# Performance work log

Hardware: AMD Instinct MI355X
Metric: run time of the kernel (lower is better)

Reference implementation:

```python
import jax, jax.numpy as jnp
import numpy as np

NUM_HEADS = 16
D_MODEL = 1024
HEAD_DIM = D_MODEL // NUM_HEADS  # 64
NEG_INF = -1e9


def alibi_bidirectional_bias(num_heads, seq_len, dtype=jnp.float32):
    """[num_heads, S, S] bias: first H/2 heads forward-causal ALiBi, last H/2 backward."""
    half = num_heads // 2
    base = 24.0 ** (1.0 / half)
    slopes = (1.0 / base ** jnp.arange(1, half + 1, dtype=dtype))[:, None, None]  # [half,1,1]
    pos = jnp.arange(seq_len)
    rel = (pos[None, :] - pos[:, None]).astype(dtype)  # rel[i,j] = j - i
    neg = jnp.full((seq_len, seq_len), NEG_INF, dtype=dtype)
    fwd = slopes * jnp.tril(rel) + jnp.triu(neg, 1)          # causal (attend past)
    bwd = slopes * jnp.triu(-rel) + jnp.tril(neg, -1)        # anti-causal (attend future)
    return jnp.concatenate([fwd, bwd], axis=0)  # [H, S, S]


def setup_inputs() -> dict:
    key = jax.random.key(0)
    ks = jax.random.split(key, 9)
    B, S, D = 2, 2048, D_MODEL
    sc = 1.0 / np.sqrt(D)
    inp = {"x": jax.random.normal(ks[0], (B, S, D), dtype=jnp.float32)}
    inp["Wq"] = jax.random.normal(ks[1], (D, D), dtype=jnp.float32) * sc
    inp["bq"] = jnp.zeros((D,), dtype=jnp.float32)
    inp["Wk"] = jax.random.normal(ks[2], (D, D), dtype=jnp.float32) * sc
    inp["bk"] = jnp.zeros((D,), dtype=jnp.float32)
    inp["Wv"] = jax.random.normal(ks[3], (D, D), dtype=jnp.float32) * sc
    inp["bv"] = jnp.zeros((D,), dtype=jnp.float32)
    inp["Wf"] = jax.random.normal(ks[4], (D, D), dtype=jnp.float32) * sc
    inp["bf"] = jnp.zeros((D,), dtype=jnp.float32)
    return inp


def reference(x, Wq, bq, Wk, bk, Wv, bv, Wf, bf):
    B, S, D = x.shape
    H, hd = NUM_HEADS, HEAD_DIM

    def heads(y):  # [B,S,D] -> [B,H,S,hd]
        return y.reshape(B, S, H, hd).transpose(0, 2, 1, 3)

    q = heads(x @ Wq + bq)
    k = heads(x @ Wk + bk)
    v = heads(x @ Wv + bv)

    bias = alibi_bidirectional_bias(H, S, x.dtype)  # [H,S,S]
    scores = jnp.einsum("bhqd,bhkd->bhqk", q, k) * (1.0 / np.sqrt(hd)) + bias[None]
    attn = jax.nn.softmax(scores, axis=-1)
    out = jnp.einsum("bhqk,bhkd->bhqd", attn, v)
    out = out.transpose(0, 2, 1, 3).reshape(B, S, D)
    return out @ Wf + bf
```

## Files before the change

kernel.cpp:

```cpp
#include <hip/hip_runtime.h>

#define S_LEN 2048
#define NH 16
#define HD 64
#define DM 1024
#define BSZ 2

typedef __bf16 bf16;
typedef __bf16 bf16x8 __attribute__((ext_vector_type(8)));
typedef float f32x4 __attribute__((ext_vector_type(4)));
typedef const unsigned int __attribute__((address_space(1)))* gas_ptr;
typedef unsigned int __attribute__((address_space(3)))* las_ptr;

__device__ __forceinline__ void gl_lds16(const bf16* g, bf16* l) {
  __builtin_amdgcn_global_load_lds((gas_ptr)g, (las_ptr)l, 16, 0, 0);
}

__global__ __launch_bounds__(256) void k_cast(const float* __restrict__ in,
                                              bf16* __restrict__ out, int n4) {
  int i = blockIdx.x * 256 + threadIdx.x;
  if (i >= n4) return;
  float4 v = ((const float4*)in)[i];
  union { ushort4 u; bf16 b[4]; } o;
  o.b[0] = (bf16)v.x; o.b[1] = (bf16)v.y; o.b[2] = (bf16)v.z; o.b[3] = (bf16)v.w;
  ((ushort4*)out)[i] = o.u;
}

__global__ __launch_bounds__(256) void k_transpose_w4(
    const float* __restrict__ W0, const float* __restrict__ W1,
    const float* __restrict__ W2, const float* __restrict__ W3,
    bf16* __restrict__ dqkv, bf16* __restrict__ df) {
  __shared__ float t[64][65];
  const int z = blockIdx.z;
  const float* W = (z == 0) ? W0 : (z == 1) ? W1 : (z == 2) ? W2 : W3;
  bf16* D = (z < 3) ? (dqkv + (size_t)z * 1048576) : df;
  int k0 = blockIdx.x * 64, n0 = blockIdx.y * 64;
  int c = threadIdx.x & 63, rr = threadIdx.x >> 6;
#pragma unroll
  for (int it = 0; it < 16; ++it) {
    int r = it * 4 + rr;
    t[r][c] = W[(size_t)(k0 + r) * DM + n0 + c];
  }
  __syncthreads();
#pragma unroll
  for (int it = 0; it < 16; ++it) {
    int r = it * 4 + rr;
    D[(size_t)(n0 + r) * DM + k0 + c] = (bf16)t[c][r];
  }
}

template <int MODE, int BM, int BN>
__global__ __launch_bounds__(256) void k_gemm(
    const bf16* __restrict__ A, const bf16* __restrict__ Bt,
    const float* __restrict__ b0, const float* __restrict__ b1,
    const float* __restrict__ b2, void* __restrict__ Cout,
    bf16* __restrict__ VtOut, int M, int N, int K) {
  __shared__ __align__(16) bf16 As[BM * 64];
  __shared__ __align__(16) bf16 Bs[BN * 64];
  constexpr int MIc = BM / 32, NIc = BN / 32;
  const int tid = threadIdx.x;
  const int l = tid & 63, w = tid >> 6;
  const int lm = l & 15, lg = l >> 4;
  const int bm = blockIdx.x * BM, bn = blockIdx.y * BN;
  const int wm = (w >> 1) * (BM / 2), wn = (w & 1) * (BN / 2);

  f32x4 acc[MIc][NIc] = {};
  const bf16* Ag = A + (size_t)bm * K;
  const bf16* Bg = Bt + (size_t)bn * K;

  for (int k0 = 0; k0 < K; k0 += 64) {
#pragma unroll
    for (int it = 0; it < BM / 32; ++it) {
      int cl = it * 256 + tid;
      int row = cl >> 3;
      int cs = ((cl & 7) ^ (row & 7)) << 3;
      gl_lds16(Ag + (size_t)row * K + k0 + cs, &As[(it * 256 + w * 64) * 8]);
    }
#pragma unroll
    for (int it = 0; it < BN / 32; ++it) {
      int cl = it * 256 + tid;
      int row = cl >> 3;
      int cs = ((cl & 7) ^ (row & 7)) << 3;
      gl_lds16(Bg + (size_t)row * K + k0 + cs, &Bs[(it * 256 + w * 64) * 8]);
    }
    __syncthreads();
#pragma unroll
    for (int kk = 0; kk < 2; ++kk) {
      bf16x8 af[MIc], bfr[NIc];
#pragma unroll
      for (int mi = 0; mi < MIc; ++mi) {
        int row = wm + mi * 16 + lm;
        af[mi] = *(const bf16x8*)&As[row * 64 + ((((kk << 2) + lg) ^ (row & 7)) << 3)];
      }
#pragma unroll
      for (int ni = 0; ni < NIc; ++ni) {
        int row = wn + ni * 16 + lm;
        bfr[ni] = *(const bf16x8*)&Bs[row * 64 + ((((kk << 2) + lg) ^ (row & 7)) << 3)];
      }
#pragma unroll
      for (int mi = 0; mi < MIc; ++mi)
#pragma unroll
        for (int ni = 0; ni < NIc; ++ni)
          acc[mi][ni] = __builtin_amdgcn_mfma_f32_16x16x32_bf16(
              af[mi], bfr[ni], acc[mi][ni], 0, 0, 0);
    }
    __syncthreads();
  }

#pragma unroll
  for (int ni = 0; ni < NIc; ++ni) {
    int n = bn + wn + ni * 16 + lm;
    float bv;
    if (MODE == 0) {
      const float* bp = (n < 1024) ? b0 : (n < 2048) ? b1 : b2;
      bv = bp[n & 1023];
    } else {
      bv = b0[n];
    }
#pragma unroll
    for (int mi = 0; mi < MIc; ++mi) {
#pragma unroll
      for (int r = 0; r < 4; ++r) {
        int m = bm + wm + mi * 16 + lg * 4 + r;
        float v = acc[mi][ni][r] + bv;
        if (MODE == 0) {
          int qkv = n >> 10;
          int h = (n >> 6) & 15;
          int d = n & 63;
          int b = m >> 11, s = m & 2047;
          if (qkv == 2) {
            VtOut[((size_t)(b * NH + h) * HD + d) * S_LEN + s] = (bf16)v;
          } else {
            ((bf16*)Cout)[(size_t)qkv * (BSZ * NH * S_LEN * HD) +
                          ((size_t)(b * NH + h) * S_LEN + s) * HD + d] = (bf16)v;
          }
        } else {
          ((float*)Cout)[(size_t)m * N + n] = v;
        }
      }
    }
  }
}

#define SMX(MASKED)                                                           \
  {                                                                           \
    const int dj = j0 - q0;                                                   \
    const float t0 = slp2 * (float)dj;                                        \
    _Pragma("unroll") for (int ni = 0; ni < 4; ++ni) {                        \
      const int koff = (ni & 1) * 32 + (ni >> 1) * 4;                         \
      float bni = t0 + dni[ni];                                               \
      float pr[4];                                                            \
      _Pragma("unroll") for (int r = 0; r < 4; ++r) {                         \
        float v = fmaf(sc[ni][r], c1, bni + srr[r]);                          \
        if (MASKED) {                                                         \
          int reli = dj + koff + relc + r;                                    \
          bool ok = causal ? (reli <= 0) : (reli >= 0);                       \
          v = ok ? v : -1e9f;                                                 \
        }                                                                     \
        pr[r] = __builtin_amdgcn_exp2f(v);                                    \
      }                                                                       \
      union { bf16 b[2]; unsigned u; } u0, u1;                                \
      u0.b[0] = (bf16)pr[0]; u0.b[1] = (bf16)pr[1];                           \
      u1.b[0] = (bf16)pr[2]; u1.b[1] = (bf16)pr[3];                           \
      pk[ni][0] = u0.u; pk[ni][1] = u1.u;                                     \
    }                                                                         \
  }

__device__ __forceinline__ void stage_kv(const bf16* __restrict__ Kp,
                                         const bf16* __restrict__ Vp,
                                         bf16* lk, bf16* lv, int j0,
                                         int w, int l) {
#pragma unroll
  for (int it = 0; it < 2; ++it) {
    const int clb = it * 256 + w * 64;
    const int cl = clb + l;
    const int row = cl >> 3, c = cl & 7;
    const int sw = (row & 3) | (((row >> 3) & 1) << 2);
    const int gc = (c ^ sw) << 3;
    gl_lds16(Kp + (size_t)(j0 + row) * HD + gc, lk + clb * 8);
    gl_lds16(Vp + (size_t)row * S_LEN + j0 + gc, lv + clb * 8);
  }
}

__global__ __launch_bounds__(256, 4) void k_attn(const bf16* __restrict__ Qh,
                                                 const bf16* __restrict__ Kh,
                                                 const bf16* __restrict__ Vt,
                                                 bf16* __restrict__ O) {
  __shared__ __align__(16) bf16 Ks[2][4096];
  __shared__ __align__(16) bf16 Vs[2][4096];
  const int id = blockIdx.x;
  const int g = id >> 3;
  const int bh = ((id & 7) << 2) | (g >> 5);
  const int yi = g & 31;
  const int b = bh >> 4, h = bh & 15;
  const bool causal = (h < 8);
  const int qb = (causal ? (31 - yi) : yi) * 64;
  const int nfull = 31 - yi;
  const int jf0 = causal ? 0 : qb + 64;
  const int w = threadIdx.x >> 6, l = threadIdx.x & 63;
  const int lm = l & 15, lg = l >> 4;
  const int q0 = qb + w * 16;
  const int hh = causal ? h : h - 8;
  const float c1 = 0.18033688f;
  const float sm = __builtin_amdgcn_exp2f(-(float)(hh + 1) * 0.57312035f) * 1.44269504f;
  const float slp2 = causal ? sm : -sm;
  const int relc = lg * 8 - lm;
  const int krow_lane = ((lm >> 2) << 3) + (lm & 3);
  const int swzK = (lm & 3) | (((lm >> 2) & 1) << 2);
  const int swzV = (lm & 3) | (((lm >> 3) & 1) << 2);
  float dni[4], srr[4];
#pragma unroll
  for (int ni = 0; ni < 4; ++ni)
    dni[ni] = slp2 * (float)((ni & 1) * 32 + (ni >> 1) * 4);
#pragma unroll
  for (int r = 0; r < 4; ++r) srr[r] = slp2 * (float)(relc + r);

  const bf16* Qp = Qh + (size_t)bh * S_LEN * HD;
  const bf16* Kp = Kh + (size_t)bh * S_LEN * HD;
  const bf16* Vp = Vt + (size_t)bh * HD * S_LEN;

  bf16x8 qf[2];
#pragma unroll
  for (int kk = 0; kk < 2; ++kk)
    qf[kk] = *(const bf16x8*)&Qp[(size_t)(q0 + lm) * HD + kk * 32 + lg * 8];
  bf16x8 ones;
#pragma unroll
  for (int i = 0; i < 8; ++i) ones[i] = (bf16)1.0f;

  f32x4 oacc[4] = {};
  f32x4 lacc = {};

  stage_kv(Kp, Vp, Ks[0], Vs[0], (0 < nfull) ? jf0 : qb, w, l);
  __syncthreads();

  for (int t = 0; t <= nfull; ++t) {
    const int cur = t & 1;
    if (t < nfull) {
      const int jn = (t + 1 < nfull) ? jf0 + (t + 1) * 64 : qb;
      stage_kv(Kp, Vp, Ks[cur ^ 1], Vs[cur ^ 1], jn, w, l);
    }
    const int j0 = (t < nfull) ? jf0 + t * 64 : qb;
    const bf16* lk = Ks[cur];
    const bf16* lv = Vs[cur];
    f32x4 sc[4] = {};
#pragma unroll
    for (int kk = 0; kk < 2; ++kk)
#pragma unroll
      for (int ni = 0; ni < 4; ++ni) {
        const int koff = (ni & 1) * 32 + (ni >> 1) * 4;
        bf16x8 kf = *(const bf16x8*)&lk[(koff + krow_lane) * 64 +
                                        ((((kk << 2) + lg) ^ swzK) << 3)];
        sc[ni] = __builtin_amdgcn_mfma_f32_16x16x32_bf16(kf, qf[kk], sc[ni], 0, 0, 0);
      }
    bf16x8 vf[2][4];
#pragma unroll
    for (int kk = 0; kk < 2; ++kk)
#pragma unroll
      for (int di = 0; di < 4; ++di)
        vf[kk][di] = *(const bf16x8*)&lv[(di * 16 + lm) * 64 +
                                         ((((kk << 2) + lg) ^ swzV) << 3)];
    unsigned pk[4][2];
    if (t == nfull) { SMX(true); } else { SMX(false); }
#pragma unroll
    for (int kk = 0; kk < 2; ++kk) {
      union { unsigned d[4]; bf16x8 v; } pa;
      pa.d[0] = pk[kk][0];
      pa.d[1] = pk[kk][1];
      pa.d[2] = pk[kk + 2][0];
      pa.d[3] = pk[kk + 2][1];
      lacc = __builtin_amdgcn_mfma_f32_16x16x32_bf16(pa.v, ones, lacc, 0, 0, 0);
#pragma unroll
      for (int di = 0; di < 4; ++di)
        oacc[di] = __builtin_amdgcn_mfma_f32_16x16x32_bf16(pa.v, vf[kk][di],
                                                           oacc[di], 0, 0, 0);
    }
    __syncthreads();
  }

  float rin[4];
#pragma unroll
  for (int r = 0; r < 4; ++r) rin[r] = 1.0f / lacc[r];
#pragma unroll
  for (int di = 0; di < 4; ++di) {
    int d = h * HD + di * 16 + lm;
#pragma unroll
    for (int r = 0; r < 4; ++r) {
      int q = q0 + lg * 4 + r;
      O[((size_t)b * S_LEN + q) * DM + d] = (bf16)(oacc[di][r] * rin[r]);
    }
  }
}

extern "C" void kernel_launch(void* const* d_in, const int* in_sizes, int n_in,
                              void* d_out, int out_size, void* d_ws, size_t ws_size,
                              hipStream_t stream) {
  const float* x  = (const float*)d_in[0];
  const float* Wq = (const float*)d_in[1];
  const float* bq = (const float*)d_in[2];
  const float* Wk = (const float*)d_in[3];
  const float* bk = (const float*)d_in[4];
  const float* Wv = (const float*)d_in[5];
  const float* bv = (const float*)d_in[6];
  const float* Wf = (const float*)d_in[7];
  const float* bfp = (const float*)d_in[8];

  char* ws = (char*)d_ws;
  const size_t MB = 1ull << 20;
  bf16* xb    = (bf16*)(ws);
  bf16* Wqkvt = (bf16*)(ws + 8 * MB);
  bf16* Wft   = (bf16*)(ws + 14 * MB);
  bf16* QKVh  = (bf16*)(ws + 16 * MB);
  bf16* Vt    = (bf16*)(ws + 40 * MB);
  bf16* O     = QKVh + 2 * 4194304;

  k_cast<<<4096, 256, 0, stream>>>(x, xb, 1048576);
  k_transpose_w4<<<dim3(16, 16, 4), 256, 0, stream>>>(Wq, Wk, Wv, Wf, Wqkvt, Wft);
  k_gemm<0, 128, 128><<<dim3(32, 24), 256, 0, stream>>>(
      xb, Wqkvt, bq, bk, bv, QKVh, Vt, 4096, 3072, 1024);
  k_attn<<<1024, 256, 0, stream>>>(QKVh, QKVh + 4194304, Vt, O);
  k_gemm<2, 64, 128><<<dim3(64, 8), 256, 0, stream>>>(
      O, Wft, bfp, bfp, bfp, d_out, nullptr, 4096, 1024, 1024);
}
```

Before: 198.4 us.

## Process paired 128-row query strips per 512-thread attention block

The attention kernel now uses 512-thread blocks (8 waves) covering 128 query rows, and each block handles two strips (pid and 15-pid) so causal and anti-causal work per block is balanced. K/V tiles are staged once per 64-key tile and shared by 8 waves instead of 4, which halves K/V load traffic per query row. Waves whose 16 rows lie entirely outside a tile skip compute but still join the barrier. The grid drops from 1024 to 256 blocks, which may lower occupancy and cause idle waves on diagonal tiles.

```diff
diff --git a/kernel.cpp b/kernel.cpp
--- a/kernel.cpp
+++ b/kernel.cpp
@@ -144,8 +144,7 @@
 
 #define SMX(MASKED)                                                           \
   {                                                                           \
-    const int dj = j0 - q0;                                                   \
-    const float t0 = slp2 * (float)dj;                                        \
+    const float t0 = slp2 * (float)dlo;                                       \
     _Pragma("unroll") for (int ni = 0; ni < 4; ++ni) {                        \
       const int koff = (ni & 1) * 32 + (ni >> 1) * 4;                         \
       float bni = t0 + dni[ni];                                               \
@@ -153,7 +152,7 @@
       _Pragma("unroll") for (int r = 0; r < 4; ++r) {                         \
         float v = fmaf(sc[ni][r], c1, bni + srr[r]);                          \
         if (MASKED) {                                                         \
-          int reli = dj + koff + relc + r;                                    \
+          int reli = dlo + koff + relc + r;                                   \
           bool ok = causal ? (reli <= 0) : (reli >= 0);                       \
           v = ok ? v : -1e9f;                                                 \
         }                                                                     \
@@ -166,40 +165,20 @@
     }                                                                         \
   }
 
-__device__ __forceinline__ void stage_kv(const bf16* __restrict__ Kp,
-                                         const bf16* __restrict__ Vp,
-                                         bf16* lk, bf16* lv, int j0,
-                                         int w, int l) {
-#pragma unroll
-  for (int it = 0; it < 2; ++it) {
-    const int clb = it * 256 + w * 64;
-    const int cl = clb + l;
-    const int row = cl >> 3, c = cl & 7;
-    const int sw = (row & 3) | (((row >> 3) & 1) << 2);
-    const int gc = (c ^ sw) << 3;
-    gl_lds16(Kp + (size_t)(j0 + row) * HD + gc, lk + clb * 8);
-    gl_lds16(Vp + (size_t)row * S_LEN + j0 + gc, lv + clb * 8);
-  }
-}
-
-__global__ __launch_bounds__(256, 4) void k_attn(const bf16* __restrict__ Qh,
+__global__ __launch_bounds__(512, 2) void k_attn(const bf16* __restrict__ Qh,
                                                  const bf16* __restrict__ Kh,
                                                  const bf16* __restrict__ Vt,
                                                  bf16* __restrict__ O) {
   __shared__ __align__(16) bf16 Ks[2][4096];
   __shared__ __align__(16) bf16 Vs[2][4096];
   const int id = blockIdx.x;
-  const int g = id >> 3;
-  const int bh = ((id & 7) << 2) | (g >> 5);
-  const int yi = g & 31;
+  const int bh = ((id & 7) << 2) | ((id >> 3) & 3);
+  const int pid = id >> 5;
   const int b = bh >> 4, h = bh & 15;
   const bool causal = (h < 8);
-  const int qb = (causal ? (31 - yi) : yi) * 64;
-  const int nfull = 31 - yi;
-  const int jf0 = causal ? 0 : qb + 64;
-  const int w = threadIdx.x >> 6, l = threadIdx.x & 63;
+  const int tid = threadIdx.x;
+  const int w = tid >> 6, l = tid & 63;
   const int lm = l & 15, lg = l >> 4;
-  const int q0 = qb + w * 16;
   const int hh = causal ? h : h - 8;
   const float c1 = 0.18033688f;
   const float sm = __builtin_amdgcn_exp2f(-(float)(hh + 1) * 0.57312035f) * 1.44269504f;
@@ -219,76 +198,99 @@
   const bf16* Kp = Kh + (size_t)bh * S_LEN * HD;
   const bf16* Vp = Vt + (size_t)bh * HD * S_LEN;
 
-  bf16x8 qf[2];
-#pragma unroll
-  for (int kk = 0; kk < 2; ++kk)
-    qf[kk] = *(const bf16x8*)&Qp[(size_t)(q0 + lm) * HD + kk * 32 + lg * 8];
   bf16x8 ones;
 #pragma unroll
   for (int i = 0; i < 8; ++i) ones[i] = (bf16)1.0f;
 
-  f32x4 oacc[4] = {};
-  f32x4 lacc = {};
-
-  stage_kv(Kp, Vp, Ks[0], Vs[0], (0 < nfull) ? jf0 : qb, w, l);
-  __syncthreads();
-
-  for (int t = 0; t <= nfull; ++t) {
-    const int cur = t & 1;
-    if (t < nfull) {
-      const int jn = (t + 1 < nfull) ? jf0 + (t + 1) * 64 : qb;
-      stage_kv(Kp, Vp, Ks[cur ^ 1], Vs[cur ^ 1], jn, w, l);
-    }
-    const int j0 = (t < nfull) ? jf0 + t * 64 : qb;
-    const bf16* lk = Ks[cur];
-    const bf16* lv = Vs[cur];
-    f32x4 sc[4] = {};
+  auto stage = [&](bf16* lk, bf16* lv, int j0) {
+    const int row = tid >> 3, c = tid & 7;
+    const int sw = (row & 3) | (((row >> 3) & 1) << 2);
+    const int gc = (c ^ sw) << 3;
+    const int clb8 = ((tid >> 6) << 6) * 8;
+    gl_lds16(Kp + (size_t)(j0 + row) * HD + gc, lk + clb8);
+    gl_lds16(Vp + (size_t)row * S_LEN + j0 + gc, lv + clb8);
+  };
+
+  auto run_strip = [&](int yi) {
+    const int qb = yi << 7;
+    const int q0 = qb + w * 16;
+    const int jbase = causal ? 0 : qb;
+    const int jcnt = causal ? (qb >> 6) + 2 : ((S_LEN - qb) >> 6);
+
+    bf16x8 qf[2];
 #pragma unroll
     for (int kk = 0; kk < 2; ++kk)
-#pragma unroll
-      for (int ni = 0; ni < 4; ++ni) {
-        const int koff = (ni & 1) * 32 + (ni >> 1) * 4;
-        bf16x8 kf = *(const bf16x8*)&lk[(koff + krow_lane) * 64 +
-                                        ((((kk << 2) + lg) ^ swzK) << 3)];
-        sc[ni] = __builtin_amdgcn_mfma_f32_16x16x32_bf16(kf, qf[kk], sc[ni], 0, 0, 0);
-      }
-    bf16x8 vf[2][4];
-#pragma unroll
-    for (int kk = 0; kk < 2; ++kk)
-#pragma unroll
-      for (int di = 0; di < 4; ++di)
-        vf[kk][di] = *(const bf16x8*)&lv[(di * 16 + lm) * 64 +
-                                         ((((kk << 2) + lg) ^ swzV) << 3)];
-    unsigned pk[4][2];
-    if (t == nfull) { SMX(true); } else { SMX(false); }
-#pragma unroll
-    for (int kk = 0; kk < 2; ++kk) {
-      union { unsigned d[4]; bf16x8 v; } pa;
-      pa.d[0] = pk[kk][0];
-      pa.d[1] = pk[kk][1];
-      pa.d[2] = pk[kk + 2][0];
-      pa.d[3] = pk[kk + 2][1];
-      lacc = __builtin_amdgcn_mfma_f32_16x16x32_bf16(pa.v, ones, lacc, 0, 0, 0);
-#pragma unroll
-      for (int di = 0; di < 4; ++di)
-        oacc[di] = __builtin_amdgcn_mfma_f32_16x16x32_bf16(pa.v, vf[kk][di],
-                                                           oacc[di], 0, 0, 0);
-    }
+      qf[kk] = *(const bf16x8*)&Qp[(size_t)(q0 + lm) * HD + kk * 32 + lg * 8];
+
+    f32x4 oacc[4] = {};
+    f32x4 lacc = {};
+
+    stage(Ks[0], Vs[0], jbase);
     __syncthreads();
-  }
-
-  float rin[4];
-#pragma unroll
-  for (int r = 0; r < 4; ++r) rin[r] = 1.0f / lacc[r];
-#pragma unroll
-  for (int di = 0; di < 4; ++di) {
-    int d = h * HD + di * 16 + lm;
-#pragma unroll
-    for (int r = 0; r < 4; ++r) {
-      int q = q0 + lg * 4 + r;
-      O[((size_t)b * S_LEN + q) * DM + d] = (bf16)(oacc[di][r] * rin[r]);
-    }
-  }
+
+    for (int t = 0; t < jcnt; ++t) {
+      const int cur = t & 1;
+      if (t + 1 < jcnt) stage(Ks[cur ^ 1], Vs[cur ^ 1], jbase + (t + 1) * 64);
+      const int j0 = jbase + t * 64;
+      const int dlo = j0 - q0;
+      const bool skip = causal ? (dlo >= 16) : (dlo <= -64);
+      if (!skip) {
+        const bf16* lk = Ks[cur];
+        const bf16* lv = Vs[cur];
+        f32x4 sc[4] = {};
+#pragma unroll
+        for (int kk = 0; kk < 2; ++kk)
+#pragma unroll
+          for (int ni = 0; ni < 4; ++ni) {
+            const int koff = (ni & 1) * 32 + (ni >> 1) * 4;
+            bf16x8 kf = *(const bf16x8*)&lk[(koff + krow_lane) * 64 +
+                                            ((((kk << 2) + lg) ^ swzK) << 3)];
+            sc[ni] = __builtin_amdgcn_mfma_f32_16x16x32_bf16(kf, qf[kk], sc[ni],
+                                                             0, 0, 0);
+          }
+        bf16x8 vf[2][4];
+#pragma unroll
+        for (int kk = 0; kk < 2; ++kk)
+#pragma unroll
+          for (int di = 0; di < 4; ++di)
+            vf[kk][di] = *(const bf16x8*)&lv[(di * 16 + lm) * 64 +
+                                             ((((kk << 2) + lg) ^ swzV) << 3)];
+        const bool full = causal ? (dlo <= -63) : (dlo >= 15);
+        unsigned pk[4][2];
+        if (full) { SMX(false); } else { SMX(true); }
+#pragma unroll
+        for (int kk = 0; kk < 2; ++kk) {
+          union { unsigned d[4]; bf16x8 v; } pa;
+          pa.d[0] = pk[kk][0];
+          pa.d[1] = pk[kk][1];
+          pa.d[2] = pk[kk + 2][0];
+          pa.d[3] = pk[kk + 2][1];
+          lacc = __builtin_amdgcn_mfma_f32_16x16x32_bf16(pa.v, ones, lacc, 0, 0, 0);
+#pragma unroll
+          for (int di = 0; di < 4; ++di)
+            oacc[di] = __builtin_amdgcn_mfma_f32_16x16x32_bf16(pa.v, vf[kk][di],
+                                                               oacc[di], 0, 0, 0);
+        }
+      }
+      __syncthreads();
+    }
+
+    float rin[4];
+#pragma unroll
+    for (int r = 0; r < 4; ++r) rin[r] = 1.0f / lacc[r];
+#pragma unroll
+    for (int di = 0; di < 4; ++di) {
+      int d = h * HD + di * 16 + lm;
+#pragma unroll
+      for (int r = 0; r < 4; ++r) {
+        int q = q0 + lg * 4 + r;
+        O[((size_t)b * S_LEN + q) * DM + d] = (bf16)(oacc[di][r] * rin[r]);
+      }
+    }
+  };
+
+  run_strip(pid);
+  run_strip(15 - pid);
 }
 
 extern "C" void kernel_launch(void* const* d_in, const int* in_sizes, int n_in,
@@ -317,7 +319,7 @@
   k_transpose_w4<<<dim3(16, 16, 4), 256, 0, stream>>>(Wq, Wk, Wv, Wf, Wqkvt, Wft);
   k_gemm<0, 128, 128><<<dim3(32, 24), 256, 0, stream>>>(
       xb, Wqkvt, bq, bk, bv, QKVh, Vt, 4096, 3072, 1024);
-  k_attn<<<1024, 256, 0, stream>>>(QKVh, QKVh + 4194304, Vt, O);
+  k_attn<<<256, 512, 0, stream>>>(QKVh, QKVh + 4194304, Vt, O);
   k_gemm<2, 64, 128><<<dim3(64, 8), 256, 0, stream>>>(
       O, Wft, bfp, bfp, bfp, d_out, nullptr, 4096, 1024, 1024);
 }
```

Result: faster. 189.7 us (-4.4%).
